# Optimization experiments

Measured on AMD Instinct MI355X. Metric: run time of the kernel, lower is better.

The kernel has to match this reference:

```python
import jax, jax.numpy as jnp
import numpy as np

N_HEAD = 100000   # head (dst/src-type) nodes
N_TAIL = 100000   # concatenated tail nodes over all edge types
E = 1600000       # total edges (avg degree 16)
IN = 128          # in_features_len (node_feature_hid_len)
OUT = 32          # out_features_len (GAT_hid_len)
NHEAD = 4
EDGE_FEATS = 32
N_ETYPES = 8
SLOPE = 0.2       # leakyrelu negative_slope


def _uniform_reset(k, shape, fan_in, fan_out):
    stdv = np.sqrt(6.0 / (fan_in + fan_out)).astype(np.float32)
    return jax.random.uniform(k, shape, jnp.float32, -stdv, stdv)


def setup_inputs() -> dict:
    key = jax.random.key(0)
    ks = jax.random.split(key, 10)
    return {
        "head_feature": jax.random.normal(ks[0], (N_HEAD, IN), jnp.float32),
        "tail_feature": jax.random.normal(ks[1], (N_TAIL, IN), jnp.float32),
        "edge_list": jax.random.randint(ks[2], (2, E), 0, N_HEAD, jnp.int32),
        "tmp_edge": jax.random.randint(ks[3], (E,), 0, N_ETYPES, jnp.int32),
        "W": _uniform_reset(ks[4], (IN, OUT * NHEAD), IN, OUT * NHEAD),
        "W_e": _uniform_reset(ks[5], (EDGE_FEATS, EDGE_FEATS * NHEAD), EDGE_FEATS, EDGE_FEATS * NHEAD),
        "a_l": _uniform_reset(ks[6], (1, NHEAD, OUT), NHEAD, OUT),
        "a_r": _uniform_reset(ks[7], (1, NHEAD, OUT), NHEAD, OUT),
        "a_e": _uniform_reset(ks[8], (1, NHEAD, EDGE_FEATS), NHEAD, EDGE_FEATS),
        "edge_emb": _uniform_reset(ks[9], (N_ETYPES, EDGE_FEATS), N_ETYPES, EDGE_FEATS),
    }


def reference(head_feature, tail_feature, edge_list, tmp_edge, W, W_e, a_l, a_r, a_e, edge_emb):
    # SimpleHGNLayer.forward (eval mode: dropouts are identity; res_attn=None;
    # first layer => node_residual=None; activation=elu).
    h_head = (head_feature @ W).reshape(-1, NHEAD, OUT)   # [N_head, H, D]
    h_tail = (tail_feature @ W).reshape(-1, NHEAD, OUT)   # [N_tail, H, D]
    e = (edge_emb @ W_e).reshape(-1, NHEAD, EDGE_FEATS)   # [T, H, De]

    head_ind = edge_list[0]
    tail_ind = edge_list[1]

    h_l = (a_l * h_head).sum(-1)[head_ind]                # [E, H]
    h_r = (a_r * h_tail).sum(-1)[tail_ind]                # [E, H]
    h_e = (a_e * e).sum(-1)[tmp_edge]                     # [E, H]
    att = jax.nn.leaky_relu(h_l + h_r + h_e, SLOPE)       # [E, H]

    # torch.sparse.softmax(dim=1) == softmax over edges sharing a head node
    m = jax.ops.segment_max(att, head_ind, num_segments=N_HEAD)       # [N_head, H]
    att_exp = jnp.exp(att - m[head_ind])
    denom = jax.ops.segment_sum(att_exp, head_ind, num_segments=N_HEAD)
    alpha = att_exp / denom[head_ind]                     # [E, H]

    # torch.sparse.mm(attn_n, h_tail[:, n, :]) for each head, vectorized
    msg = alpha[:, :, None] * h_tail[tail_ind]            # [E, H, D]
    out = jax.ops.segment_sum(msg, head_ind, num_segments=N_HEAD)     # [N_head, H, D]
    out = out.reshape(N_HEAD, NHEAD * OUT)
    return jax.nn.elu(out)
```

## Files before the change

### kernel.cpp

```cpp
#include <hip/hip_runtime.h>
#include <hip/hip_bf16.h>
#include <hip/hip_fp16.h>
#include <math.h>

#define N_HEADN 100000
#define N_TAILN 100000
#define NEDGE   1600000
#define SLOPE   0.2f

#define NB   196
#define HPB  512
#define BCAP 9216

static __device__ __forceinline__ float bf2f(__hip_bfloat16 x) { return __bfloat162float(x); }

#define FMA_MIX_LO(acc, pk, q) \
  asm("v_fma_mix_f32 %0, %1, %2, %0 op_sel_hi:[1,0,0]" : "+v"(acc) : "v"(pk), "v"(q))
#define FMA_MIX_HI(acc, pk, q) \
  asm("v_fma_mix_f32 %0, %1, %2, %0 op_sel:[1,0,0] op_sel_hi:[1,0,0]" : "+v"(acc) : "v"(pk), "v"(q))

__global__ __launch_bounds__(256) void k0m(const float* __restrict__ W,
                                           const float* __restrict__ W_e,
                                           const float* __restrict__ a_l,
                                           const float* __restrict__ a_e,
                                           const float* __restrict__ emb,
                                           __hip_bfloat16* __restrict__ Wb,
                                           float* __restrict__ wl,
                                           float* __restrict__ he) {
  const int i = (blockIdx.x * 256 + threadIdx.x) * 4;
  const float4 v = *(const float4*)&W[i];
  union { unsigned short us[4]; uint2 u2; } pk;
  __hip_bfloat16 b0 = __float2bfloat16(v.x); pk.us[0] = *(unsigned short*)&b0;
  __hip_bfloat16 b1 = __float2bfloat16(v.y); pk.us[1] = *(unsigned short*)&b1;
  __hip_bfloat16 b2 = __float2bfloat16(v.z); pk.us[2] = *(unsigned short*)&b2;
  __hip_bfloat16 b3 = __float2bfloat16(v.w); pk.us[3] = *(unsigned short*)&b3;
  *(uint2*)&Wb[i] = pk.u2;
  if (blockIdx.x == 0 && threadIdx.x < 128) {
    const int t = threadIdx.x;
    #pragma unroll
    for (int h = 0; h < 4; ++h) {
      float sl = 0.f;
      for (int d = 0; d < 32; ++d)
        sl += W[t * 128 + h * 32 + d] * a_l[h * 32 + d];
      wl[t * 4 + h] = sl;
    }
    if (t < 32) {
      const int et = t >> 2, h = t & 3;
      float acc = 0.f;
      for (int d = 0; d < 32; ++d) {
        float tmp = 0.f;
        for (int f = 0; f < 32; ++f)
          tmp += emb[et * 32 + f] * W_e[f * 128 + h * 32 + d];
        acc += a_e[h * 32 + d] * tmp;
      }
      he[et * 4 + h] = acc;
    }
  }
}

__global__ __launch_bounds__(256) void k1_hlr(const float* __restrict__ feat,
                                              const float* __restrict__ wv,
                                              float* __restrict__ o) {
  const int gid = blockIdx.x * 256 + threadIdx.x;
  const int node = gid >> 4, li = gid & 15;
  const float4* row = (const float4*)(feat + (size_t)node * 128 + li * 8);
  const float4 x0 = row[0], x1 = row[1];
  const float* w = wv + li * 32;
  float p0 = 0.f, p1 = 0.f, p2 = 0.f, p3 = 0.f;
  const float xs[8] = {x0.x, x0.y, x0.z, x0.w, x1.x, x1.y, x1.z, x1.w};
  #pragma unroll
  for (int j = 0; j < 8; ++j) {
    const float4 wj = *(const float4*)&w[j * 4];
    p0 += xs[j] * wj.x;
    p1 += xs[j] * wj.y;
    p2 += xs[j] * wj.z;
    p3 += xs[j] * wj.w;
  }
  #pragma unroll
  for (int m = 8; m; m >>= 1) {
    p0 += __shfl_xor(p0, m, 64);
    p1 += __shfl_xor(p1, m, 64);
    p2 += __shfl_xor(p2, m, 64);
    p3 += __shfl_xor(p3, m, 64);
  }
  if (li == 0) *(float4*)(o + (size_t)node * 4) = make_float4(p0, p1, p2, p3);
}

__global__ __launch_bounds__(256) void k2_gemm(const float* __restrict__ A,
                                               const __hip_bfloat16* __restrict__ Wb,
                                               const float* __restrict__ a_r,
                                               __half* __restrict__ out,
                                               float* __restrict__ h_r) {
  __shared__ __hip_bfloat16 sW[128 * 128];
  __shared__ __hip_bfloat16 sA[128 * 68];
  const int t = threadIdx.x;
  {
    const uint4* src = (const uint4*)Wb;
    uint4* dst = (uint4*)sW;
    #pragma unroll
    for (int i = 0; i < 8; ++i) dst[i * 256 + t] = src[i * 256 + t];
  }
  const int r0 = blockIdx.x * 64;
  #pragma unroll
  for (int ii = 0; ii < 8; ++ii) {
    const int i = ii * 256 + t;
    const int r = i >> 5, k4 = (i & 31) * 4;
    float4 v = make_float4(0.f, 0.f, 0.f, 0.f);
    if (r0 + r < N_TAILN) v = *(const float4*)&A[(size_t)(r0 + r) * 128 + k4];
    sA[(k4 + 0) * 68 + r] = __float2bfloat16(v.x);
    sA[(k4 + 1) * 68 + r] = __float2bfloat16(v.y);
    sA[(k4 + 2) * 68 + r] = __float2bfloat16(v.z);
    sA[(k4 + 3) * 68 + r] = __float2bfloat16(v.w);
  }
  __syncthreads();

  const int tc = t & 15, tr = t >> 4;
  const int c8 = tc * 8, r4 = tr * 4;
  float acc[4][8];
  #pragma unroll
  for (int i = 0; i < 4; ++i)
    #pragma unroll
    for (int j = 0; j < 8; ++j) acc[i][j] = 0.f;

  #pragma unroll 2
  for (int k = 0; k < 128; ++k) {
    const uint2 ab = *(const uint2*)&sA[k * 68 + r4];
    const float ar[4] = {__uint_as_float(ab.x << 16), __uint_as_float(ab.x & 0xffff0000u),
                         __uint_as_float(ab.y << 16), __uint_as_float(ab.y & 0xffff0000u)};
    const uint4 wbv = *(const uint4*)&sW[k * 128 + c8];
    float w[8];
    w[0] = __uint_as_float(wbv.x << 16); w[1] = __uint_as_float(wbv.x & 0xffff0000u);
    w[2] = __uint_as_float(wbv.y << 16); w[3] = __uint_as_float(wbv.y & 0xffff0000u);
    w[4] = __uint_as_float(wbv.z << 16); w[5] = __uint_as_float(wbv.z & 0xffff0000u);
    w[6] = __uint_as_float(wbv.w << 16); w[7] = __uint_as_float(wbv.w & 0xffff0000u);
    #pragma unroll
    for (int i = 0; i < 4; ++i)
      #pragma unroll
      for (int j = 0; j < 8; ++j)
        acc[i][j] += ar[i] * w[j];
  }

  const int hh = tc >> 2, d0 = (tc & 3) * 8;
  const float4 ar0 = *(const float4*)&a_r[hh * 32 + d0];
  const float4 ar1 = *(const float4*)&a_r[hh * 32 + d0 + 4];
  #pragma unroll
  for (int i = 0; i < 4; ++i) {
    float hr = acc[i][0] * ar0.x + acc[i][1] * ar0.y + acc[i][2] * ar0.z + acc[i][3] * ar0.w
             + acc[i][4] * ar1.x + acc[i][5] * ar1.y + acc[i][6] * ar1.z + acc[i][7] * ar1.w;
    hr += __shfl_xor(hr, 1, 64);
    hr += __shfl_xor(hr, 2, 64);
    if ((tc & 3) == 0 && (r0 + r4 + i) < N_TAILN)
      h_r[(size_t)(r0 + r4 + i) * 4 + hh] = hr;
  }

  #pragma unroll
  for (int i = 0; i < 4; ++i) {
    const int rr = r0 + r4 + i;
    if (rr < N_TAILN) {
      union { unsigned short us[8]; uint4 u4; } pk;
      #pragma unroll
      for (int j = 0; j < 8; ++j) {
        __half b = __float2half(acc[i][j]);
        pk.us[j] = *(unsigned short*)&b;
      }
      *(uint4*)&out[(size_t)rr * 128 + c8] = pk.u4;
    }
  }
}

__global__ __launch_bounds__(256) void p1_part(const int* __restrict__ head_ind,
                                               const int* __restrict__ tail_ind,
                                               const int* __restrict__ etype,
                                               int* __restrict__ bucketCursor,
                                               unsigned int* __restrict__ recs) {
  __shared__ int hist[NB];
  const int t = threadIdx.x;
  for (int i = t; i < NB; i += 256) hist[i] = 0;
  __syncthreads();
  const int e0 = blockIdx.x * 6400;
  int h[25];
  #pragma unroll
  for (int i = 0; i < 25; ++i) {
    h[i] = head_ind[e0 + i * 256 + t];
    atomicAdd(&hist[h[i] >> 9], 1);
  }
  __syncthreads();
  for (int i = t; i < NB; i += 256) {
    const int c = hist[i];
    hist[i] = atomicAdd(&bucketCursor[i], c);
  }
  __syncthreads();
  #pragma unroll
  for (int i = 0; i < 25; ++i) {
    const int e = e0 + i * 256 + t;
    const int hi = h[i];
    const int b = hi >> 9;
    const int pos = atomicAdd(&hist[b], 1);
    recs[b * BCAP + pos] = (unsigned)tail_ind[e] | ((unsigned)etype[e] << 17)
                         | ((unsigned)(hi & 511) << 20);
  }
}

__global__ __launch_bounds__(256) void p2_off(const unsigned int* __restrict__ recs,
                                              const int* __restrict__ bucketCursor,
                                              int* __restrict__ off) {
  __shared__ int hist[HPB];
  __shared__ int red[256];
  const int b = blockIdx.x, t = threadIdx.x;
  red[t] = (t < b) ? bucketCursor[t] : 0;
  for (int i = t; i < HPB; i += 256) hist[i] = 0;
  __syncthreads();
  for (int st = 128; st; st >>= 1) {
    if (t < st) red[t] += red[t + st];
    __syncthreads();
  }
  const int bstart = red[0];
  const int cnt = bucketCursor[b];
  for (int i = t; i < cnt; i += 256)
    atomicAdd(&hist[recs[b * BCAP + i] >> 20], 1);
  __syncthreads();
  const int o0 = hist[t], o1 = hist[t + 256];
  for (int st = 1; st < 512; st <<= 1) {
    const int v0 = (t >= st) ? hist[t - st] : 0;
    const int v1 = (t + 256 >= st) ? hist[t + 256 - st] : 0;
    __syncthreads();
    hist[t] += v0;
    hist[t + 256] += v1;
    __syncthreads();
  }
  const int h0 = b * HPB;
  if (h0 + t < N_HEADN)       off[h0 + t] = bstart + hist[t] - o0;
  if (h0 + 256 + t < N_HEADN) off[h0 + 256 + t] = bstart + hist[t + 256] - o1;
  if (b == NB - 1 && t == 0)  off[N_HEADN] = NEDGE;
}

__global__ __launch_bounds__(256) void p3_scatter(const unsigned int* __restrict__ recs,
                                                  const int* __restrict__ bucketCursor,
                                                  const int* __restrict__ off,
                                                  int* __restrict__ pt) {
  __shared__ int cur[HPB];
  const int b = blockIdx.x, t = threadIdx.x;
  const int h0 = b * HPB;
  for (int i = t; i < HPB; i += 256)
    cur[i] = (h0 + i < N_HEADN) ? off[h0 + i] : 0;
  __syncthreads();
  const int cnt = bucketCursor[b];
  for (int i = t; i < cnt; i += 256) {
    const unsigned r = recs[b * BCAP + i];
    const int pos = atomicAdd(&cur[r >> 20], 1);
    pt[pos] = (int)(r & 0xFFFFFu);
  }
}

__global__ __launch_bounds__(256) void k4_agg(const int* __restrict__ off,
                                              const int* __restrict__ pt,
                                              const float* __restrict__ h_l,
                                              const float* __restrict__ h_r,
                                              const float* __restrict__ he,
                                              const __half* __restrict__ h_tail,
                                              float* __restrict__ out) {
  __shared__ __align__(16) float sw[4][4][72];
  __shared__ int sti[4][4][20];
  __shared__ __align__(16) float4 she4[8];
  const int wid = threadIdx.x >> 6;
  const int lane = threadIdx.x & 63;
  const int g = lane >> 4, li = lane & 15;
  if (threadIdx.x < 8) she4[threadIdx.x] = ((const float4*)he)[threadIdx.x];
  __syncthreads();
  const int n = blockIdx.x * 16 + wid * 4 + g;
  const int s = off[n], e = off[n + 1];
  const int nch = (e - s + 15) >> 4;
  const float4 hl = *(const float4*)(h_l + (size_t)n * 4);
  const int h = li >> 2;
  const unsigned dby = (unsigned)li * 16u;
  float m0 = -1e30f, m1 = -1e30f, m2 = -1e30f, m3 = -1e30f;
  float s0 = 0.f, s1 = 0.f, s2 = 0.f, s3 = 0.f;
  float acc[8];
  #pragma unroll
  for (int d = 0; d < 8; ++d) acc[d] = 0.f;
  float* __restrict__ swg = &sw[wid][g][0];
  int* __restrict__ stig = &sti[wid][g][0];
  const char* __restrict__ htb = (const char*)h_tail;
  for (int c = 0; c < nch; ++c) {
    const int base = s + (c << 4);
    const int rem = min(16, e - base);
    float a0 = -1e30f, a1 = -1e30f, a2 = -1e30f, a3 = -1e30f;
    if (li < rem) {
      const int pk = pt[base + li];
      const unsigned ti = (unsigned)pk & 0x1FFFFu;
      const int et = (pk >> 17) & 7;
      const float4 hr = *(const float4*)((const char*)h_r + (ti << 4));
      const float4 hv = she4[et];
      a0 = hl.x + hr.x + hv.x;
      a1 = hl.y + hr.y + hv.y;
      a2 = hl.z + hr.z + hv.z;
      a3 = hl.w + hr.w + hv.w;
      a0 = fmaxf(a0, SLOPE * a0);
      a1 = fmaxf(a1, SLOPE * a1);
      a2 = fmaxf(a2, SLOPE * a2);
      a3 = fmaxf(a3, SLOPE * a3);
      stig[li] = (int)(ti << 8);
    }
    float c0 = a0, c1 = a1, c2 = a2, c3 = a3;
    #pragma unroll
    for (int msk = 8; msk; msk >>= 1) {
      c0 = fmaxf(c0, __shfl_xor(c0, msk, 64));
      c1 = fmaxf(c1, __shfl_xor(c1, msk, 64));
      c2 = fmaxf(c2, __shfl_xor(c2, msk, 64));
      c3 = fmaxf(c3, __shfl_xor(c3, msk, 64));
    }
    const float nm0 = fmaxf(m0, c0), nm1 = fmaxf(m1, c1);
    const float nm2 = fmaxf(m2, c2), nm3 = fmaxf(m3, c3);
    const float e0 = __expf(m0 - nm0), e1 = __expf(m1 - nm1);
    const float e2 = __expf(m2 - nm2), e3 = __expf(m3 - nm3);
    const float w0 = __expf(a0 - nm0), w1 = __expf(a1 - nm1);
    const float w2 = __expf(a2 - nm2), w3 = __expf(a3 - nm3);
    float t0 = w0, t1 = w1, t2 = w2, t3 = w3;
    #pragma unroll
    for (int msk = 8; msk; msk >>= 1) {
      t0 += __shfl_xor(t0, msk, 64);
      t1 += __shfl_xor(t1, msk, 64);
      t2 += __shfl_xor(t2, msk, 64);
      t3 += __shfl_xor(t3, msk, 64);
    }
    s0 = s0 * e0 + t0; s1 = s1 * e1 + t1;
    s2 = s2 * e2 + t2; s3 = s3 * e3 + t3;
    m0 = nm0; m1 = nm1; m2 = nm2; m3 = nm3;
    *(float4*)&swg[li * 4] = make_float4(w0, w1, w2, w3);
    const float sc = (h == 0) ? e0 : (h == 1) ? e1 : (h == 2) ? e2 : e3;
    #pragma unroll
    for (int d = 0; d < 8; ++d) acc[d] *= sc;
    __builtin_amdgcn_wave_barrier();
    int j = 0;
    for (; j + 4 <= rem; j += 4) {
      const int o0 = stig[j], o1 = stig[j + 1], o2 = stig[j + 2], o3 = stig[j + 3];
      const float q0 = swg[(j + 0) * 4 + h];
      const float q1 = swg[(j + 1) * 4 + h];
      const float q2 = swg[(j + 2) * 4 + h];
      const float q3 = swg[(j + 3) * 4 + h];
      const uint4 v0 = *(const uint4*)(htb + (unsigned)o0 + dby);
      const uint4 v1 = *(const uint4*)(htb + (unsigned)o1 + dby);
      const uint4 v2 = *(const uint4*)(htb + (unsigned)o2 + dby);
      const uint4 v3 = *(const uint4*)(htb + (unsigned)o3 + dby);
      FMA_MIX_LO(acc[0], v0.x, q0); FMA_MIX_HI(acc[1], v0.x, q0);
      FMA_MIX_LO(acc[2], v0.y, q0); FMA_MIX_HI(acc[3], v0.y, q0);
      FMA_MIX_LO(acc[4], v0.z, q0); FMA_MIX_HI(acc[5], v0.z, q0);
      FMA_MIX_LO(acc[6], v0.w, q0); FMA_MIX_HI(acc[7], v0.w, q0);
      FMA_MIX_LO(acc[0], v1.x, q1); FMA_MIX_HI(acc[1], v1.x, q1);
      FMA_MIX_LO(acc[2], v1.y, q1); FMA_MIX_HI(acc[3], v1.y, q1);
      FMA_MIX_LO(acc[4], v1.z, q1); FMA_MIX_HI(acc[5], v1.z, q1);
      FMA_MIX_LO(acc[6], v1.w, q1); FMA_MIX_HI(acc[7], v1.w, q1);
      FMA_MIX_LO(acc[0], v2.x, q2); FMA_MIX_HI(acc[1], v2.x, q2);
      FMA_MIX_LO(acc[2], v2.y, q2); FMA_MIX_HI(acc[3], v2.y, q2);
      FMA_MIX_LO(acc[4], v2.z, q2); FMA_MIX_HI(acc[5], v2.z, q2);
      FMA_MIX_LO(acc[6], v2.w, q2); FMA_MIX_HI(acc[7], v2.w, q2);
      FMA_MIX_LO(acc[0], v3.x, q3); FMA_MIX_HI(acc[1], v3.x, q3);
      FMA_MIX_LO(acc[2], v3.y, q3); FMA_MIX_HI(acc[3], v3.y, q3);
      FMA_MIX_LO(acc[4], v3.z, q3); FMA_MIX_HI(acc[5], v3.z, q3);
      FMA_MIX_LO(acc[6], v3.w, q3); FMA_MIX_HI(acc[7], v3.w, q3);
    }
    for (; j < rem; ++j) {
      const int o = stig[j];
      const float q = swg[j * 4 + h];
      const uint4 v = *(const uint4*)(htb + (unsigned)o + dby);
      FMA_MIX_LO(acc[0], v.x, q); FMA_MIX_HI(acc[1], v.x, q);
      FMA_MIX_LO(acc[2], v.y, q); FMA_MIX_HI(acc[3], v.y, q);
      FMA_MIX_LO(acc[4], v.z, q); FMA_MIX_HI(acc[5], v.z, q);
      FMA_MIX_LO(acc[6], v.w, q); FMA_MIX_HI(acc[7], v.w, q);
    }
    __builtin_amdgcn_wave_barrier();
  }
  const float denom = (h == 0) ? s0 : (h == 1) ? s1 : (h == 2) ? s2 : s3;
  const float inv = denom > 0.f ? 1.f / denom : 0.f;
  float o[8];
  #pragma unroll
  for (int d = 0; d < 8; ++d) {
    const float v = acc[d] * inv;
    o[d] = v > 0.f ? v : expm1f(v);
  }
  float* op = out + (size_t)n * 128 + li * 8;
  *(float4*)op = make_float4(o[0], o[1], o[2], o[3]);
  *(float4*)(op + 4) = make_float4(o[4], o[5], o[6], o[7]);
}

extern "C" void kernel_launch(void* const* d_in, const int* in_sizes, int n_in,
                              void* d_out, int out_size, void* d_ws, size_t ws_size,
                              hipStream_t stream) {
  const float* head = (const float*)d_in[0];
  const float* tail = (const float*)d_in[1];
  const int* elist  = (const int*)d_in[2];
  const int* etype  = (const int*)d_in[3];
  const float* W    = (const float*)d_in[4];
  const float* W_e  = (const float*)d_in[5];
  const float* a_l  = (const float*)d_in[6];
  const float* a_r  = (const float*)d_in[7];
  const float* a_e  = (const float*)d_in[8];
  const float* emb  = (const float*)d_in[9];
  const int* head_ind = elist;
  const int* tail_ind = elist + NEDGE;
  (void)in_sizes; (void)n_in; (void)out_size; (void)ws_size;

  char* p = (char*)d_ws;
  size_t o = 0;
  auto carve = [&](size_t bytes) {
    char* r = p + o;
    o += (bytes + 255) & ~(size_t)255;
    return r;
  };
  __half* h_tail = (__half*)carve((size_t)N_TAILN * 128 * 2);
  int*   pt     = (int*)   carve((size_t)NEDGE * 4);
  unsigned int* recs = (unsigned int*)carve((size_t)NB * BCAP * 4);
  float* h_l    = (float*) carve((size_t)N_HEADN * 4 * 4);
  float* h_r    = (float*) carve((size_t)N_TAILN * 4 * 4);
  int*   off    = (int*)   carve((size_t)(N_HEADN + 1) * 4);
  int*   bucketCursor = (int*)carve(NB * 4);
  float* wl     = (float*) carve(128 * 4 * 4);
  float* he     = (float*) carve(8 * 4 * 4);
  __hip_bfloat16* Wb = (__hip_bfloat16*)carve(16384 * 2);

  hipMemsetAsync(bucketCursor, 0, NB * sizeof(int), stream);
  k0m<<<16, 256, 0, stream>>>(W, W_e, a_l, a_e, emb, Wb, wl, he);
  k1_hlr<<<(N_HEADN * 16) / 256, 256, 0, stream>>>(head, wl, h_l);
  k2_gemm<<<(N_TAILN + 63) / 64, 256, 0, stream>>>(tail, Wb, a_r, h_tail, h_r);
  p1_part<<<NEDGE / 6400, 256, 0, stream>>>(head_ind, tail_ind, etype, bucketCursor, recs);
  p2_off<<<NB, 256, 0, stream>>>(recs, bucketCursor, off);
  p3_scatter<<<NB, 256, 0, stream>>>(recs, bucketCursor, off, pt);
  k4_agg<<<N_HEADN / 16, 256, 0, stream>>>(off, pt, h_l, h_r, he, h_tail, (float*)d_out);
}
```

Baseline: 363.0 us.

## Fuse offset and scatter passes, shrink partition blocks for more parallelism

The per-bucket offset computation and scatter kernels are merged into one 1024-thread kernel that keeps running cursors in shared memory, dropping a launch and a global round-trip of the offsets. The partition kernel now handles 1280 edges per block instead of 6400, giving 1250 blocks rather than 250 so the GPU is better filled. It also skips global atomics on empty bucket counts. The trade-off is more blocks doing global atomics on the bucket cursors, which adds contention.

```diff
diff --git a/kernel.cpp b/kernel.cpp
--- a/kernel.cpp
+++ b/kernel.cpp
@@ -177,21 +177,21 @@
   const int t = threadIdx.x;
   for (int i = t; i < NB; i += 256) hist[i] = 0;
   __syncthreads();
-  const int e0 = blockIdx.x * 6400;
-  int h[25];
-  #pragma unroll
-  for (int i = 0; i < 25; ++i) {
+  const int e0 = blockIdx.x * 1280;
+  int h[5];
+  #pragma unroll
+  for (int i = 0; i < 5; ++i) {
     h[i] = head_ind[e0 + i * 256 + t];
     atomicAdd(&hist[h[i] >> 9], 1);
   }
   __syncthreads();
   for (int i = t; i < NB; i += 256) {
     const int c = hist[i];
-    hist[i] = atomicAdd(&bucketCursor[i], c);
-  }
-  __syncthreads();
-  #pragma unroll
-  for (int i = 0; i < 25; ++i) {
+    hist[i] = (c > 0) ? atomicAdd(&bucketCursor[i], c) : 0;
+  }
+  __syncthreads();
+  #pragma unroll
+  for (int i = 0; i < 5; ++i) {
     const int e = e0 + i * 256 + t;
     const int hi = h[i];
     const int b = hi >> 9;
@@ -201,14 +201,15 @@
   }
 }
 
-__global__ __launch_bounds__(256) void p2_off(const unsigned int* __restrict__ recs,
-                                              const int* __restrict__ bucketCursor,
-                                              int* __restrict__ off) {
-  __shared__ int hist[HPB];
+__global__ __launch_bounds__(1024) void p23(const unsigned int* __restrict__ recs,
+                                            const int* __restrict__ bucketCursor,
+                                            int* __restrict__ off,
+                                            int* __restrict__ pt) {
+  __shared__ int cur[HPB];
   __shared__ int red[256];
   const int b = blockIdx.x, t = threadIdx.x;
-  red[t] = (t < b) ? bucketCursor[t] : 0;
-  for (int i = t; i < HPB; i += 256) hist[i] = 0;
+  if (t < 256) red[t] = (t < b) ? bucketCursor[t] : 0;
+  if (t < HPB) cur[t] = 0;
   __syncthreads();
   for (int st = 128; st; st >>= 1) {
     if (t < st) red[t] += red[t + st];
@@ -216,37 +217,28 @@
   }
   const int bstart = red[0];
   const int cnt = bucketCursor[b];
-  for (int i = t; i < cnt; i += 256)
-    atomicAdd(&hist[recs[b * BCAP + i] >> 20], 1);
-  __syncthreads();
-  const int o0 = hist[t], o1 = hist[t + 256];
-  for (int st = 1; st < 512; st <<= 1) {
-    const int v0 = (t >= st) ? hist[t - st] : 0;
-    const int v1 = (t + 256 >= st) ? hist[t + 256 - st] : 0;
+  const unsigned int* __restrict__ rb = recs + (size_t)b * BCAP;
+  for (int i = t; i < cnt; i += 1024)
+    atomicAdd(&cur[rb[i] >> 20], 1);
+  __syncthreads();
+  const int orig = (t < HPB) ? cur[t] : 0;
+  for (int st = 1; st < HPB; st <<= 1) {
+    int v = 0;
+    if (t < HPB && t >= st) v = cur[t - st];
     __syncthreads();
-    hist[t] += v0;
-    hist[t + 256] += v1;
+    if (t < HPB) cur[t] += v;
     __syncthreads();
   }
   const int h0 = b * HPB;
-  if (h0 + t < N_HEADN)       off[h0 + t] = bstart + hist[t] - o0;
-  if (h0 + 256 + t < N_HEADN) off[h0 + 256 + t] = bstart + hist[t + 256] - o1;
-  if (b == NB - 1 && t == 0)  off[N_HEADN] = NEDGE;
-}
-
-__global__ __launch_bounds__(256) void p3_scatter(const unsigned int* __restrict__ recs,
-                                                  const int* __restrict__ bucketCursor,
-                                                  const int* __restrict__ off,
-                                                  int* __restrict__ pt) {
-  __shared__ int cur[HPB];
-  const int b = blockIdx.x, t = threadIdx.x;
-  const int h0 = b * HPB;
-  for (int i = t; i < HPB; i += 256)
-    cur[i] = (h0 + i < N_HEADN) ? off[h0 + i] : 0;
-  __syncthreads();
-  const int cnt = bucketCursor[b];
-  for (int i = t; i < cnt; i += 256) {
-    const unsigned r = recs[b * BCAP + i];
+  if (t < HPB) {
+    const int excl = bstart + cur[t] - orig;
+    cur[t] = excl;
+    if (h0 + t < N_HEADN) off[h0 + t] = excl;
+  }
+  if (b == NB - 1 && t == 0) off[N_HEADN] = NEDGE;
+  __syncthreads();
+  for (int i = t; i < cnt; i += 1024) {
+    const unsigned r = rb[i];
     const int pos = atomicAdd(&cur[r >> 20], 1);
     pt[pos] = (int)(r & 0xFFFFFu);
   }
@@ -422,8 +414,7 @@
   k0m<<<16, 256, 0, stream>>>(W, W_e, a_l, a_e, emb, Wb, wl, he);
   k1_hlr<<<(N_HEADN * 16) / 256, 256, 0, stream>>>(head, wl, h_l);
   k2_gemm<<<(N_TAILN + 63) / 64, 256, 0, stream>>>(tail, Wb, a_r, h_tail, h_r);
-  p1_part<<<NEDGE / 6400, 256, 0, stream>>>(head_ind, tail_ind, etype, bucketCursor, recs);
-  p2_off<<<NB, 256, 0, stream>>>(recs, bucketCursor, off);
-  p3_scatter<<<NB, 256, 0, stream>>>(recs, bucketCursor, off, pt);
+  p1_part<<<NEDGE / 1280, 256, 0, stream>>>(head_ind, tail_ind, etype, bucketCursor, recs);
+  p23<<<NB, 1024, 0, stream>>>(recs, bucketCursor, off, pt);
   k4_agg<<<N_HEADN / 16, 256, 0, stream>>>(off, pt, h_l, h_r, he, h_tail, (float*)d_out);
 }
```

Result: no change. 364.4 us (+0.4%).
